# Kernel optimization log

Hardware: AMD Instinct MI355X
Metric: run time of the kernel (lower is better)

## Reference

```python
import jax, jax.numpy as jnp
import numpy as np

B, T = 32768, 32
OBJ_V, PRED_V = 179, 46
E_OBJ, E_PRED, H = 5, 5, 32
IN_DIM = E_OBJ + E_PRED + 2 + 4  # 16, matches LSTMCell input size


def setup_inputs() -> dict:
    key = jax.random.key(0)
    ks = jax.random.split(key, 12)
    s = 0.1
    return {
        "input_objects": jax.random.randint(ks[0], (B, T), 0, OBJ_V),
        "input_boxes": jax.random.uniform(ks[1], (B, T, 4), dtype=jnp.float32),
        "predicates": jax.random.randint(ks[2], (B, T), 0, PRED_V),
        "subject_indicators": jax.random.randint(ks[3], (B, T), 0, 2),
        "target_object": jax.random.randint(ks[4], (B,), 0, OBJ_V),
        "obj_emb": jax.random.normal(ks[5], (OBJ_V, E_OBJ), dtype=jnp.float32) * s,
        "pred_emb": jax.random.normal(ks[6], (PRED_V, E_PRED), dtype=jnp.float32) * s,
        "W_ih": jax.random.normal(ks[7], (4 * H, IN_DIM), dtype=jnp.float32) * s,
        "W_hh": jax.random.normal(ks[8], (4 * H, H), dtype=jnp.float32) * s,
        "b_ih": jnp.zeros((4 * H,), dtype=jnp.float32),
        "b_hh": jnp.zeros((4 * H,), dtype=jnp.float32),
        "fc2_W": jax.random.normal(ks[9], (4, H), dtype=jnp.float32) * s,
        "fc2_b": jnp.zeros((4,), dtype=jnp.float32),
    }


def _forward(input_objects, input_boxes, predicates, subject_indicators,
             obj_emb, pred_emb, W_ih, W_hh, b_ih, b_hh, fc2_W, fc2_b):
    # concatenate_features, vectorized over all timesteps at once: [B,T,16]
    feats = jnp.concatenate([
        obj_emb[input_objects],                                   # [B,T,5]
        pred_emb[predicates],                                     # [B,T,5]
        jax.nn.one_hot(subject_indicators, 2, dtype=jnp.float32), # [B,T,2]
        input_boxes,                                              # [B,T,4]
    ], axis=-1)
    xs = jnp.transpose(feats, (1, 0, 2))  # [T,B,16] for scan over time

    def step(carry, x):
        h, c = carry
        gates = x @ W_ih.T + b_ih + h @ W_hh.T + b_hh  # [B,4H]
        i, f, g, o = jnp.split(gates, 4, axis=-1)      # torch gate order i,f,g,o
        i = jax.nn.sigmoid(i)
        f = jax.nn.sigmoid(f)
        g = jnp.tanh(g)
        o = jax.nn.sigmoid(o)
        c = f * c + i * g
        h = o * jnp.tanh(c)
        return (h, c), None

    h0 = jnp.zeros((input_objects.shape[0], H), dtype=jnp.float32)
    (h, _), _ = jax.lax.scan(step, (h0, h0), xs)
    out = h @ fc2_W.T + fc2_b          # output_fc2 on last hidden state
    return jnp.clip(out, 0.0, 1.0)     # torch.clamp(min=0, max=1)


def reference(input_objects, input_boxes, predicates, subject_indicators, target_object,
              obj_emb, pred_emb, W_ih, W_hh, b_ih, b_hh, fc2_W, fc2_b):
    # target_object is accepted by the torch forward but unused in its body
    return _forward(input_objects, input_boxes, predicates, subject_indicators,
                    obj_emb, pred_emb, W_ih, W_hh, b_ih, b_hh, fc2_W, fc2_b)
```

## Files before the change

kernel.cpp:

```cpp
#include <hip/hip_runtime.h>

#define LDS_BYTES 18720

typedef _Float16 f16x8 __attribute__((ext_vector_type(8)));
typedef __fp16   fp16x2 __attribute__((ext_vector_type(2)));
typedef float    f32x4 __attribute__((ext_vector_type(4)));
typedef float    f32x2 __attribute__((ext_vector_type(2)));

#define LOG2E     1.44269504088896f
#define TWO_LOG2E 2.88539008177793f

__global__ __launch_bounds__(256, 8)
void lstm_fused(const int* __restrict__ objs,
                const float* __restrict__ boxes,
                const int* __restrict__ preds,
                const int* __restrict__ subj,
                const float* __restrict__ obj_emb,
                const float* __restrict__ pred_emb,
                const float* __restrict__ W_ih,
                const float* __restrict__ W_hh,
                const float* __restrict__ b_ih,
                const float* __restrict__ b_hh,
                const float* __restrict__ fc2_W,
                const float* __restrict__ fc2_b,
                float* __restrict__ out)
{
    extern __shared__ char smem[];
    const int tid  = threadIdx.x;
    const int lane = tid & 63;
    const int wv   = tid >> 6;
    const int quad = lane >> 4;
    const int cidx = lane & 15;
    const int XOFF = 0, HX0 = 16640, HX1 = 17664, ZOFF = 18688;

    if (tid < 8) ((int*)(smem + ZOFF))[tid] = 0;

    {
        int b  = tid >> 4;
        int t0 = (tid & 15) << 1;
        long gb = (long)blockIdx.x * 16 + b;
        int2 ov = *(const int2*)(objs  + gb * 32 + t0);
        int2 pv = *(const int2*)(preds + gb * 32 + t0);
        int2 sv = *(const int2*)(subj  + gb * 32 + t0);
        int oarr[2] = {ov.x, ov.y};
        int parr[2] = {pv.x, pv.y};
        int sarr[2] = {sv.x, sv.y};
        #pragma unroll
        for (int tt = 0; tt < 2; ++tt) {
            int t = t0 + tt;
            const float* eo = obj_emb  + oarr[tt] * 5;
            const float* ep = pred_emb + parr[tt] * 5;
            float4 bx = *(const float4*)(boxes + (gb * 32 + t) * 4);
            f16x8 lo, hi;
            lo[0]=(_Float16)eo[0]; lo[1]=(_Float16)eo[1]; lo[2]=(_Float16)eo[2];
            lo[3]=(_Float16)eo[3]; lo[4]=(_Float16)eo[4];
            lo[5]=(_Float16)ep[0]; lo[6]=(_Float16)ep[1]; lo[7]=(_Float16)ep[2];
            hi[0]=(_Float16)ep[3]; hi[1]=(_Float16)ep[4];
            hi[2]=(_Float16)(sarr[tt]==0 ? 1.0f : 0.0f);
            hi[3]=(_Float16)(sarr[tt]==1 ? 1.0f : 0.0f);
            hi[4]=(_Float16)bx.x; hi[5]=(_Float16)bx.y;
            hi[6]=(_Float16)bx.z; hi[7]=(_Float16)bx.w;
            char* dst = smem + XOFF + b * 1040 + t * 32;
            *(f16x8*)dst        = lo;
            *(f16x8*)(dst + 16) = hi;
        }
    }

    f16x8 Wf[2][2];
    f32x4 bias4[2];
    #pragma unroll
    for (int tile = 0; tile < 2; ++tile) {
        int rm   = cidx & 3;
        int u    = 8 * (cidx >> 2) + 2 * wv + (rm & 1);
        int gate = tile * 2 + (rm >> 1);
        float scale = (gate == 2) ? TWO_LOG2E : -LOG2E;
        int n = gate * 32 + u;
        #pragma unroll
        for (int ks = 0; ks < 2; ++ks) {
            f16x8 v;
            #pragma unroll
            for (int jj = 0; jj < 8; ++jj) {
                int k = ks * 32 + quad * 8 + jj;
                float val = (k < 16) ? W_ih[n * 16 + k]
                          : (k >= 32) ? W_hh[n * 32 + (k - 32)]
                          : 0.0f;
                v[jj] = (_Float16)(val * scale);
            }
            Wf[tile][ks] = v;
        }
        #pragma unroll
        for (int r = 0; r < 4; ++r) {
            int ur = 8 * quad + 2 * wv + (r & 1);
            int gr = tile * 2 + (r >> 1);
            float sc = (gr == 2) ? TWO_LOG2E : -LOG2E;
            bias4[tile][r] = (b_ih[gr * 32 + ur] + b_hh[gr * 32 + ur]) * sc;
        }
    }

    const bool qlow = (quad < 2);
    int       xaddr = qlow ? (XOFF + cidx * 1040 + quad * 16) : ZOFF;
    const int xinc  = qlow ? 32 : 0;
    const int slot16 = lane << 4;
    const int wr_off = slot16 + (wv << 2);

    __syncthreads();

    f16x8 xfrag = *(const f16x8*)(smem + xaddr); xaddr += xinc;
    f32x4 accp[2];
    #pragma unroll
    for (int tile = 0; tile < 2; ++tile)
        accp[tile] = __builtin_amdgcn_mfma_f32_16x16x32_f16(Wf[tile][0], xfrag, bias4[tile], 0, 0, 0);

    union { int i[4]; f16x8 v; } hf;
    hf.i[0] = 0; hf.i[1] = 0; hf.i[2] = 0; hf.i[3] = 0;
    const f32x2 one = {1.0f, 1.0f};
    f32x2 cstv = {0.0f, 0.0f};
    f32x2 hv = {0.0f, 0.0f};

    #pragma unroll
    for (int t = 0; t < 32; ++t) {
        f32x4 acc0 = __builtin_amdgcn_mfma_f32_16x16x32_f16(Wf[0][1], hf.v, accp[0], 0, 0, 0);
        f32x4 acc1 = __builtin_amdgcn_mfma_f32_16x16x32_f16(Wf[1][1], hf.v, accp[1], 0, 0, 0);

        f16x8 xn = *(const f16x8*)(smem + xaddr); xaddr += xinc;

        f32x2 Ei = {__builtin_amdgcn_exp2f(acc0[0]), __builtin_amdgcn_exp2f(acc0[1])};
        f32x2 Ef = {__builtin_amdgcn_exp2f(acc0[2]), __builtin_amdgcn_exp2f(acc0[3])};
        f32x2 Eg = {__builtin_amdgcn_exp2f(acc1[0]), __builtin_amdgcn_exp2f(acc1[1])};
        f32x2 Eo = {__builtin_amdgcn_exp2f(acc1[2]), __builtin_amdgcn_exp2f(acc1[3])};

        f32x2 t1  = Ei + one;
        f32x2 dig = t1 * Eg + t1;
        f32x2 tf  = Ef + one;
        f32x2 nn  = (Eg - one) * tf + cstv * dig;
        f32x2 den = tf * dig;
        f32x2 rde = {__builtin_amdgcn_rcpf(den.x), __builtin_amdgcn_rcpf(den.y)};
        f32x2 c   = nn * rde;
        cstv = c;
        f32x2 cl  = c * TWO_LOG2E;
        f32x2 Ec  = {__builtin_amdgcn_exp2f(cl.x), __builtin_amdgcn_exp2f(cl.y)};
        f32x2 to  = Eo + one;
        f32x2 dh  = to * Ec + to;
        f32x2 rdh = {__builtin_amdgcn_rcpf(dh.x), __builtin_amdgcn_rcpf(dh.y)};
        hv = (Ec - one) * rdh;

        union { fp16x2 h; int i; } pku;
        pku.h = __builtin_amdgcn_cvt_pkrtz(hv.x, hv.y);

        char* buf = smem + ((t & 1) ? HX1 : HX0);
        *(int*)(buf + wr_off) = pku.i;
        __syncthreads();

        hf.v = *(const f16x8*)(buf + slot16);

        accp[0] = __builtin_amdgcn_mfma_f32_16x16x32_f16(Wf[0][0], xn, bias4[0], 0, 0, 0);
        accp[1] = __builtin_amdgcn_mfma_f32_16x16x32_f16(Wf[1][0], xn, bias4[1], 0, 0, 0);
    }

    __syncthreads();
    {
        int u0 = 8 * quad + 2 * wv;
        *(float2*)(smem + cidx * 144 + u0 * 4) = (float2){hv.x, hv.y};
    }
    __syncthreads();

    if (tid < 64) {
        int b = tid >> 2, jj = tid & 3;
        const float* fw   = fc2_W + jj * 32;
        const float* hrow = (const float*)(smem + b * 144);
        float s = fc2_b[jj];
        #pragma unroll
        for (int k = 0; k < 8; ++k) {
            float4 hvv = *(const float4*)(hrow + k * 4);
            s += fw[k*4+0] * hvv.x + fw[k*4+1] * hvv.y
               + fw[k*4+2] * hvv.z + fw[k*4+3] * hvv.w;
        }
        s = fminf(fmaxf(s, 0.0f), 1.0f);
        out[(long)blockIdx.x * 64 + tid] = s;
    }
}

extern "C" void kernel_launch(void* const* d_in, const int* in_sizes, int n_in,
                              void* d_out, int out_size, void* d_ws, size_t ws_size,
                              hipStream_t stream)
{
    lstm_fused<<<2048, 256, LDS_BYTES, stream>>>(
        (const int*)d_in[0], (const float*)d_in[1], (const int*)d_in[2],
        (const int*)d_in[3],
        (const float*)d_in[5], (const float*)d_in[6],
        (const float*)d_in[7], (const float*)d_in[8],
        (const float*)d_in[9], (const float*)d_in[10],
        (const float*)d_in[11], (const float*)d_in[12],
        (float*)d_out);
}
```

Baseline: 128.7 us.

## Run each 16-sequence LSTM block in a single wavefront without per-step barriers

Each block now has one 64-lane wavefront instead of four. That wavefront computes all 128 gate rows with 8 MFMA tiles per step, and the weight row layout is arranged so each lane's outputs form its own h fragment for the next step. This removes the per-timestep LDS write, __syncthreads and LDS read of the hidden state. In exchange there is 4x more serial work per wave, more registers, and fewer waves per CU for hiding latency. The LDS row stride is also padded, presumably to avoid bank conflicts.

After: 129.0 us. About the same (+0.2%).

```diff
diff --git a/kernel.cpp b/kernel.cpp
--- a/kernel.cpp
+++ b/kernel.cpp
@@ -1,6 +1,8 @@
 #include <hip/hip_runtime.h>
 
-#define LDS_BYTES 18720
+#define XSTRIDE 1072
+#define ZOFF    (16 * XSTRIDE)
+#define LDS_BYTES (ZOFF + 32)
 
 typedef _Float16 f16x8 __attribute__((ext_vector_type(8)));
 typedef __fp16   fp16x2 __attribute__((ext_vector_type(2)));
@@ -10,7 +12,7 @@
 #define LOG2E     1.44269504088896f
 #define TWO_LOG2E 2.88539008177793f
 
-__global__ __launch_bounds__(256, 8)
+__global__ __launch_bounds__(64, 2)
 void lstm_fused(const int* __restrict__ objs,
                 const float* __restrict__ boxes,
                 const int* __restrict__ preds,
@@ -26,157 +28,166 @@
                 float* __restrict__ out)
 {
     extern __shared__ char smem[];
-    const int tid  = threadIdx.x;
-    const int lane = tid & 63;
-    const int wv   = tid >> 6;
+    const int lane = threadIdx.x;
     const int quad = lane >> 4;
     const int cidx = lane & 15;
-    const int XOFF = 0, HX0 = 16640, HX1 = 17664, ZOFF = 18688;
-
-    if (tid < 8) ((int*)(smem + ZOFF))[tid] = 0;
+
+    if (lane < 8) ((int*)(smem + ZOFF))[lane] = 0;
 
     {
-        int b  = tid >> 4;
-        int t0 = (tid & 15) << 1;
-        long gb = (long)blockIdx.x * 16 + b;
-        int2 ov = *(const int2*)(objs  + gb * 32 + t0);
-        int2 pv = *(const int2*)(preds + gb * 32 + t0);
-        int2 sv = *(const int2*)(subj  + gb * 32 + t0);
-        int oarr[2] = {ov.x, ov.y};
-        int parr[2] = {pv.x, pv.y};
-        int sarr[2] = {sv.x, sv.y};
-        #pragma unroll
-        for (int tt = 0; tt < 2; ++tt) {
-            int t = t0 + tt;
-            const float* eo = obj_emb  + oarr[tt] * 5;
-            const float* ep = pred_emb + parr[tt] * 5;
-            float4 bx = *(const float4*)(boxes + (gb * 32 + t) * 4);
+        const int b = lane >> 2;
+        const int j = lane & 3;
+        const long gb = (long)blockIdx.x * 16 + b;
+        const int* orow = objs + gb * 32;
+        const int* prow = preds + gb * 32;
+        const int* srow = subj + gb * 32;
+        const float* brow = boxes + gb * 128;
+        char* xrow = smem + b * XSTRIDE;
+        #pragma unroll
+        for (int tt = 0; tt < 8; ++tt) {
+            int t = j + tt * 4;
+            int o = orow[t], p = prow[t], sv = srow[t];
+            const float* eo = obj_emb + o * 5;
+            const float* ep = pred_emb + p * 5;
+            float4 bx = *(const float4*)(brow + t * 4);
             f16x8 lo, hi;
             lo[0]=(_Float16)eo[0]; lo[1]=(_Float16)eo[1]; lo[2]=(_Float16)eo[2];
             lo[3]=(_Float16)eo[3]; lo[4]=(_Float16)eo[4];
             lo[5]=(_Float16)ep[0]; lo[6]=(_Float16)ep[1]; lo[7]=(_Float16)ep[2];
             hi[0]=(_Float16)ep[3]; hi[1]=(_Float16)ep[4];
-            hi[2]=(_Float16)(sarr[tt]==0 ? 1.0f : 0.0f);
-            hi[3]=(_Float16)(sarr[tt]==1 ? 1.0f : 0.0f);
+            hi[2]=(_Float16)(sv==0 ? 1.0f : 0.0f);
+            hi[3]=(_Float16)(sv==1 ? 1.0f : 0.0f);
             hi[4]=(_Float16)bx.x; hi[5]=(_Float16)bx.y;
             hi[6]=(_Float16)bx.z; hi[7]=(_Float16)bx.w;
-            char* dst = smem + XOFF + b * 1040 + t * 32;
-            *(f16x8*)dst        = lo;
-            *(f16x8*)(dst + 16) = hi;
-        }
-    }
-
-    f16x8 Wf[2][2];
-    f32x4 bias4[2];
+            *(f16x8*)(xrow + t * 32)      = lo;
+            *(f16x8*)(xrow + t * 32 + 16) = hi;
+        }
+    }
+
+    f16x8 WH[8], WX[8];
+    f32x4 bias[8];
     #pragma unroll
-    for (int tile = 0; tile < 2; ++tile) {
-        int rm   = cidx & 3;
-        int u    = 8 * (cidx >> 2) + 2 * wv + (rm & 1);
-        int gate = tile * 2 + (rm >> 1);
-        float scale = (gate == 2) ? TWO_LOG2E : -LOG2E;
-        int n = gate * 32 + u;
-        #pragma unroll
-        for (int ks = 0; ks < 2; ++ks) {
-            f16x8 v;
+    for (int a = 0; a < 8; ++a) {
+        const int gate = a >> 1;
+        const float scale = (gate == 2) ? TWO_LOG2E : -LOG2E;
+        const int n = gate * 32 + 8 * (cidx >> 2) + 4 * (a & 1) + (cidx & 3);
+        const float* wr = W_hh + n * 32 + quad * 8;
+        float4 w0 = *(const float4*)(wr);
+        float4 w1 = *(const float4*)(wr + 4);
+        f16x8 h8;
+        h8[0]=(_Float16)(w0.x*scale); h8[1]=(_Float16)(w0.y*scale);
+        h8[2]=(_Float16)(w0.z*scale); h8[3]=(_Float16)(w0.w*scale);
+        h8[4]=(_Float16)(w1.x*scale); h8[5]=(_Float16)(w1.y*scale);
+        h8[6]=(_Float16)(w1.z*scale); h8[7]=(_Float16)(w1.w*scale);
+        WH[a] = h8;
+        f16x8 x8;
+        if (quad < 2) {
+            const float* xr = W_ih + n * 16 + quad * 8;
+            float4 u0 = *(const float4*)(xr);
+            float4 u1 = *(const float4*)(xr + 4);
+            x8[0]=(_Float16)(u0.x*scale); x8[1]=(_Float16)(u0.y*scale);
+            x8[2]=(_Float16)(u0.z*scale); x8[3]=(_Float16)(u0.w*scale);
+            x8[4]=(_Float16)(u1.x*scale); x8[5]=(_Float16)(u1.y*scale);
+            x8[6]=(_Float16)(u1.z*scale); x8[7]=(_Float16)(u1.w*scale);
+        } else {
             #pragma unroll
-            for (int jj = 0; jj < 8; ++jj) {
-                int k = ks * 32 + quad * 8 + jj;
-                float val = (k < 16) ? W_ih[n * 16 + k]
-                          : (k >= 32) ? W_hh[n * 32 + (k - 32)]
-                          : 0.0f;
-                v[jj] = (_Float16)(val * scale);
-            }
-            Wf[tile][ks] = v;
-        }
-        #pragma unroll
-        for (int r = 0; r < 4; ++r) {
-            int ur = 8 * quad + 2 * wv + (r & 1);
-            int gr = tile * 2 + (r >> 1);
-            float sc = (gr == 2) ? TWO_LOG2E : -LOG2E;
-            bias4[tile][r] = (b_ih[gr * 32 + ur] + b_hh[gr * 32 + ur]) * sc;
-        }
-    }
+            for (int jj = 0; jj < 8; ++jj) x8[jj] = (_Float16)0.0f;
+        }
+        WX[a] = x8;
+        const int nb = gate * 32 + 8 * quad + 4 * (a & 1);
+        float4 bi = *(const float4*)(b_ih + nb);
+        float4 bh = *(const float4*)(b_hh + nb);
+        f32x4 bb = {(bi.x+bh.x)*scale, (bi.y+bh.y)*scale,
+                    (bi.z+bh.z)*scale, (bi.w+bh.w)*scale};
+        bias[a] = bb;
+    }
+
+    __syncthreads();
 
     const bool qlow = (quad < 2);
-    int       xaddr = qlow ? (XOFF + cidx * 1040 + quad * 16) : ZOFF;
-    const int xinc  = qlow ? 32 : 0;
-    const int slot16 = lane << 4;
-    const int wr_off = slot16 + (wv << 2);
-
-    __syncthreads();
+    int xaddr = qlow ? (cidx * XSTRIDE + quad * 16) : ZOFF;
+    const int xinc = qlow ? 32 : 0;
 
     f16x8 xfrag = *(const f16x8*)(smem + xaddr); xaddr += xinc;
-    f32x4 accp[2];
+    f32x4 accp[8];
     #pragma unroll
-    for (int tile = 0; tile < 2; ++tile)
-        accp[tile] = __builtin_amdgcn_mfma_f32_16x16x32_f16(Wf[tile][0], xfrag, bias4[tile], 0, 0, 0);
+    for (int a = 0; a < 8; ++a)
+        accp[a] = __builtin_amdgcn_mfma_f32_16x16x32_f16(WX[a], xfrag, bias[a], 0, 0, 0);
 
     union { int i[4]; f16x8 v; } hf;
-    hf.i[0] = 0; hf.i[1] = 0; hf.i[2] = 0; hf.i[3] = 0;
+    hf.i[0]=0; hf.i[1]=0; hf.i[2]=0; hf.i[3]=0;
+    const f32x2 zz = {0.0f, 0.0f};
+    f32x2 cst[4] = {zz, zz, zz, zz};
+    f32x2 hv[4];
     const f32x2 one = {1.0f, 1.0f};
-    f32x2 cstv = {0.0f, 0.0f};
-    f32x2 hv = {0.0f, 0.0f};
-
-    #pragma unroll
+
+    #pragma unroll 4
     for (int t = 0; t < 32; ++t) {
-        f32x4 acc0 = __builtin_amdgcn_mfma_f32_16x16x32_f16(Wf[0][1], hf.v, accp[0], 0, 0, 0);
-        f32x4 acc1 = __builtin_amdgcn_mfma_f32_16x16x32_f16(Wf[1][1], hf.v, accp[1], 0, 0, 0);
+        f32x4 acc[8];
+        #pragma unroll
+        for (int a = 0; a < 8; ++a)
+            acc[a] = __builtin_amdgcn_mfma_f32_16x16x32_f16(WH[a], hf.v, accp[a], 0, 0, 0);
 
         f16x8 xn = *(const f16x8*)(smem + xaddr); xaddr += xinc;
 
-        f32x2 Ei = {__builtin_amdgcn_exp2f(acc0[0]), __builtin_amdgcn_exp2f(acc0[1])};
-        f32x2 Ef = {__builtin_amdgcn_exp2f(acc0[2]), __builtin_amdgcn_exp2f(acc0[3])};
-        f32x2 Eg = {__builtin_amdgcn_exp2f(acc1[0]), __builtin_amdgcn_exp2f(acc1[1])};
-        f32x2 Eo = {__builtin_amdgcn_exp2f(acc1[2]), __builtin_amdgcn_exp2f(acc1[3])};
-
-        f32x2 t1  = Ei + one;
-        f32x2 dig = t1 * Eg + t1;
-        f32x2 tf  = Ef + one;
-        f32x2 nn  = (Eg - one) * tf + cstv * dig;
-        f32x2 den = tf * dig;
-        f32x2 rde = {__builtin_amdgcn_rcpf(den.x), __builtin_amdgcn_rcpf(den.y)};
-        f32x2 c   = nn * rde;
-        cstv = c;
-        f32x2 cl  = c * TWO_LOG2E;
-        f32x2 Ec  = {__builtin_amdgcn_exp2f(cl.x), __builtin_amdgcn_exp2f(cl.y)};
-        f32x2 to  = Eo + one;
-        f32x2 dh  = to * Ec + to;
-        f32x2 rdh = {__builtin_amdgcn_rcpf(dh.x), __builtin_amdgcn_rcpf(dh.y)};
-        hv = (Ec - one) * rdh;
-
-        union { fp16x2 h; int i; } pku;
-        pku.h = __builtin_amdgcn_cvt_pkrtz(hv.x, hv.y);
-
-        char* buf = smem + ((t & 1) ? HX1 : HX0);
-        *(int*)(buf + wr_off) = pku.i;
-        __syncthreads();
-
-        hf.v = *(const f16x8*)(buf + slot16);
-
-        accp[0] = __builtin_amdgcn_mfma_f32_16x16x32_f16(Wf[0][0], xn, bias4[0], 0, 0, 0);
-        accp[1] = __builtin_amdgcn_mfma_f32_16x16x32_f16(Wf[1][0], xn, bias4[1], 0, 0, 0);
+        #pragma unroll
+        for (int cc = 0; cc < 4; ++cc) {
+            const int sel = cc >> 1;
+            const int r0  = (cc & 1) << 1;
+            f32x2 zi = {acc[0+sel][r0], acc[0+sel][r0+1]};
+            f32x2 zf = {acc[2+sel][r0], acc[2+sel][r0+1]};
+            f32x2 zg = {acc[4+sel][r0], acc[4+sel][r0+1]};
+            f32x2 zo = {acc[6+sel][r0], acc[6+sel][r0+1]};
+            f32x2 Ei = {__builtin_amdgcn_exp2f(zi.x), __builtin_amdgcn_exp2f(zi.y)};
+            f32x2 Ef = {__builtin_amdgcn_exp2f(zf.x), __builtin_amdgcn_exp2f(zf.y)};
+            f32x2 Eg = {__builtin_amdgcn_exp2f(zg.x), __builtin_amdgcn_exp2f(zg.y)};
+            f32x2 Eo = {__builtin_amdgcn_exp2f(zo.x), __builtin_amdgcn_exp2f(zo.y)};
+            f32x2 t1  = Ei + one;
+            f32x2 dig = t1 * Eg + t1;
+            f32x2 tf  = Ef + one;
+            f32x2 nn  = (Eg - one) * tf + cst[cc] * dig;
+            f32x2 den = tf * dig;
+            f32x2 rde = {__builtin_amdgcn_rcpf(den.x), __builtin_amdgcn_rcpf(den.y)};
+            f32x2 c   = nn * rde;
+            cst[cc] = c;
+            f32x2 cl  = c * TWO_LOG2E;
+            f32x2 Ec  = {__builtin_amdgcn_exp2f(cl.x), __builtin_amdgcn_exp2f(cl.y)};
+            f32x2 to  = Eo + one;
+            f32x2 dh  = to * Ec + to;
+            f32x2 rdh = {__builtin_amdgcn_rcpf(dh.x), __builtin_amdgcn_rcpf(dh.y)};
+            hv[cc] = (Ec - one) * rdh;
+            union { fp16x2 h; int i; } pk;
+            pk.h = __builtin_amdgcn_cvt_pkrtz(hv[cc].x, hv[cc].y);
+            hf.i[cc] = pk.i;
+        }
+
+        #pragma unroll
+        for (int a = 0; a < 8; ++a)
+            accp[a] = __builtin_amdgcn_mfma_f32_16x16x32_f16(WX[a], xn, bias[a], 0, 0, 0);
     }
 
     __syncthreads();
     {
-        int u0 = 8 * quad + 2 * wv;
-        *(float2*)(smem + cidx * 144 + u0 * 4) = (float2){hv.x, hv.y};
+        char* s0 = smem + cidx * 144 + quad * 32;
+        float4 lo4 = {hv[0].x, hv[0].y, hv[1].x, hv[1].y};
+        float4 hi4 = {hv[2].x, hv[2].y, hv[3].x, hv[3].y};
+        *(float4*)s0        = lo4;
+        *(float4*)(s0 + 16) = hi4;
     }
     __syncthreads();
-
-    if (tid < 64) {
-        int b = tid >> 2, jj = tid & 3;
-        const float* fw   = fc2_W + jj * 32;
+    {
+        const int b = lane >> 2, j = lane & 3;
         const float* hrow = (const float*)(smem + b * 144);
-        float s = fc2_b[jj];
+        const float* fw = fc2_W + j * 32;
+        float s = fc2_b[j];
         #pragma unroll
         for (int k = 0; k < 8; ++k) {
             float4 hvv = *(const float4*)(hrow + k * 4);
-            s += fw[k*4+0] * hvv.x + fw[k*4+1] * hvv.y
-               + fw[k*4+2] * hvv.z + fw[k*4+3] * hvv.w;
+            float4 wv4 = *(const float4*)(fw + k * 4);
+            s += wv4.x*hvv.x + wv4.y*hvv.y + wv4.z*hvv.z + wv4.w*hvv.w;
         }
         s = fminf(fmaxf(s, 0.0f), 1.0f);
-        out[(long)blockIdx.x * 64 + tid] = s;
+        out[(long)blockIdx.x * 64 + lane] = s;
     }
 }
 
@@ -184,7 +195,7 @@
                               void* d_out, int out_size, void* d_ws, size_t ws_size,
                               hipStream_t stream)
 {
-    lstm_fused<<<2048, 256, LDS_BYTES, stream>>>(
+    lstm_fused<<<2048, 64, LDS_BYTES, stream>>>(
         (const int*)d_in[0], (const float*)d_in[1], (const int*)d_in[2],
         (const int*)d_in[3],
         (const float*)d_in[5], (const float*)d_in[6],
```
